# Performance work log

Hardware: AMD Instinct MI355X
Metric: run time of the kernel (lower is better)

Reference implementation:

```python
import jax, jax.numpy as jnp
import numpy as np

N, E, DIN, H, DOUT, NBLK = 50000, 300000, 963, 256, 3, 6


def gconv(x, src, dst, ew, W, Wl, b):
    # support = x @ W ; out[i] = sum_j ew_ij * support[j] + x[i] @ W_loop + b
    sup = x @ W
    agg = jax.ops.segment_sum(ew[:, None] * sup[src], dst, num_segments=N)
    return agg + x @ Wl + b


def setup_inputs() -> dict:
    key = jax.random.key(0)
    ks = jax.random.split(key, 16)
    s = 0.05
    x = jax.random.normal(ks[0], (N, DIN), jnp.float32)
    src = jax.random.randint(ks[1], (E,), 0, N, dtype=jnp.int32)
    dst = jax.random.randint(ks[2], (E,), 0, N, dtype=jnp.int32)
    ew = jax.random.uniform(ks[3], (E,), jnp.float32)
    W1 = jax.random.normal(ks[4], (DIN, H), jnp.float32) * s
    Wl1 = jax.random.normal(ks[5], (DIN, H), jnp.float32) * s
    b1 = jnp.zeros((H,), jnp.float32)
    # stacked residual-block weights: [NBLK, 2 convs, H, H]
    blkW = jax.random.normal(ks[6], (NBLK, 2, H, H), jnp.float32) * s
    blkWl = jax.random.normal(ks[7], (NBLK, 2, H, H), jnp.float32) * s
    blkb = jnp.zeros((NBLK, 2, H), jnp.float32)
    W2 = jax.random.normal(ks[8], (H, DOUT), jnp.float32) * s
    Wl2 = jax.random.normal(ks[9], (H, DOUT), jnp.float32) * s
    b2 = jnp.zeros((DOUT,), jnp.float32)
    return dict(x=x, src=src, dst=dst, ew=ew, W1=W1, Wl1=Wl1, b1=b1,
                blkW=blkW, blkWl=blkWl, blkb=blkb, W2=W2, Wl2=Wl2, b2=b2)


def reference(x, src, dst, ew, W1, Wl1, b1, blkW, blkWl, blkb, W2, Wl2, b2):
    h = jax.nn.relu(gconv(x, src, dst, ew, W1, Wl1, b1))

    def block(h, p):
        W, Wl, b = p  # W: [2,H,H]
        y = jax.nn.relu(gconv(h, src, dst, ew, W[0], Wl[0], b[0]))
        y = jax.nn.relu(gconv(y, src, dst, ew, W[1], Wl[1], b[1]))
        return (h + y) * 0.5, None

    x_hidden, _ = jax.lax.scan(block, h, (blkW, blkWl, blkb))
    x_out = gconv(x_hidden, src, dst, ew, W2, Wl2, b2)
    return (x_out, x_hidden)
```

## Files before the change

kernel.cpp:

```cpp
#include <hip/hip_runtime.h>

typedef __attribute__((ext_vector_type(8))) short short8;
typedef __attribute__((ext_vector_type(4))) float f32x4;

constexpr int kN = 50000;
constexpr int kE = 300000;
constexpr int kDIN = 963;
constexpr int kH = 256;
constexpr int kNBLK = 6;

__device__ inline unsigned short f2bf(float f) {
    unsigned u = __float_as_uint(f);
    u = u + 0x7FFFu + ((u >> 16) & 1u);
    return (unsigned short)(u >> 16);
}
__device__ inline float bf2f(unsigned short s) {
    return __uint_as_float(((unsigned)s) << 16);
}

__device__ inline void gload_lds16(const void* g, void* l) {
    __builtin_amdgcn_global_load_lds(
        (const __attribute__((address_space(1))) void*)g,
        (__attribute__((address_space(3))) void*)l, 16, 0, 0);
}

template<bool ACVT>
__global__ __launch_bounds__(512) void gemm_dual(
    const void* __restrict__ Av, const unsigned short* __restrict__ Bt,
    const float* __restrict__ bias,
    unsigned short* __restrict__ supb, unsigned short* __restrict__ tpreb,
    int M, int Kpad, int Kvalid, int Astride)
{
    __shared__ __align__(16) char smem[49152];
    char* As = smem;
    char* Bs = smem + 16384;

    const int tid = threadIdx.x;
    const int wid = tid >> 6;
    const int lane = tid & 63;
    const int wr = wid >> 2, wc = wid & 3;

    const int nwg = gridDim.x;
    const int q = nwg >> 3, r = nwg & 7;
    const int xcd = blockIdx.x & 7, idx = blockIdx.x >> 3;
    const int t = (xcd < r ? xcd * (q + 1) : r * (q + 1) + (xcd - r) * q) + idx;
    const int r0 = (t >> 1) * 128;
    const int c0 = (t & 1) * 256;

    f32x4 acc[4][4];
#pragma unroll
    for (int i = 0; i < 4; ++i)
#pragma unroll
        for (int j = 0; j < 4; ++j) acc[i][j] = f32x4{0.f, 0.f, 0.f, 0.f};

    const int l_row = lane >> 3;
    const int l_c   = lane & 7;

    for (int k0 = 0; k0 < Kpad; k0 += 64) {
#pragma unroll
        for (int p = 0; p < 4; ++p) {
            int row = wid * 32 + p * 8 + l_row;
            int csw = l_c ^ (row & 7);
            const unsigned short* g = Bt + (long)(c0 + row) * Kpad + k0 + csw * 8;
            gload_lds16(g, Bs + (wid * 32 + p * 8) * 128);
        }
        if (!ACVT) {
            const unsigned short* A = (const unsigned short*)Av;
#pragma unroll
            for (int p = 0; p < 2; ++p) {
                int row = wid * 16 + p * 8 + l_row;
                int grow = r0 + row; if (grow >= M) grow = M - 1;
                int csw = l_c ^ (row & 7);
                const unsigned short* g = A + (long)grow * Astride + k0 + csw * 8;
                gload_lds16(g, As + (wid * 16 + p * 8) * 128);
            }
        } else {
            const int row = tid >> 2;
            const int kq = tid & 3;
            int grow = r0 + row; if (grow >= M) grow = M - 1;
            const float* ar = (const float*)Av + (long)grow * Astride;
#pragma unroll
            for (int j = 0; j < 2; ++j) {
                int k16 = kq * 2 + j;
                short8 v;
#pragma unroll
                for (int ii = 0; ii < 8; ++ii) {
                    int k = k0 + k16 * 8 + ii;
                    float f = (k < Kvalid) ? ar[k] : 0.f;
                    v[ii] = (short)f2bf(f);
                }
                *(short8*)(As + row * 128 + ((k16 ^ (row & 7)) << 4)) = v;
            }
        }
        __syncthreads();

#pragma unroll
        for (int kk = 0; kk < 2; ++kk) {
            short8 af[4], bfr[4];
            const int kg = kk * 4 + (lane >> 4);
#pragma unroll
            for (int nr = 0; nr < 4; ++nr) {
                int row = wr * 64 + nr * 16 + (lane & 15);
                af[nr] = *(const short8*)(As + row * 128 + ((kg ^ (row & 7)) << 4));
            }
#pragma unroll
            for (int mc = 0; mc < 4; ++mc) {
                int row = wc * 64 + mc * 16 + (lane & 15);
                bfr[mc] = *(const short8*)(Bs + row * 128 + ((kg ^ (row & 7)) << 4));
            }
#pragma unroll
            for (int mc = 0; mc < 4; ++mc)
#pragma unroll
                for (int nr = 0; nr < 4; ++nr)
                    acc[mc][nr] = __builtin_amdgcn_mfma_f32_16x16x32_bf16(
                        bfr[mc], af[nr], acc[mc][nr], 0, 0, 0);
        }
        __syncthreads();
    }

    const bool isSup = (c0 == 0);
    unsigned short* outp = isSup ? supb : tpreb;
    float* eL = (float*)smem;
    const int wrow = wr * 16 + (lane & 15);
    const int qc = (lane >> 4) << 2;

    for (int nr = 0; nr < 4; ++nr) {
        __syncthreads();
#pragma unroll
        for (int mc = 0; mc < 4; ++mc) {
            const int col = wc * 64 + mc * 16 + qc;
            f32x4 v = acc[mc][nr];
            if (!isSup) v += *(const f32x4*)(bias + col);
            const int c16 = col >> 2;
            *(f32x4*)(eL + wrow * 256 + ((c16 ^ wrow) << 2)) = v;
        }
        __syncthreads();
        const int tr = tid >> 4, j = tid & 15;
        const int gr = r0 + (tr >> 4) * 64 + nr * 16 + (tr & 15);
        if (gr < M) {
#pragma unroll
            for (int p = 0; p < 2; ++p) {
                const int u = j + 16 * p;
                f32x4 lo = *(const f32x4*)(eL + tr * 256 + (((2 * u) ^ tr) << 2));
                f32x4 hi = *(const f32x4*)(eL + tr * 256 + (((2 * u + 1) ^ tr) << 2));
                uint4 pk;
                pk.x = (unsigned)f2bf(lo[0]) | ((unsigned)f2bf(lo[1]) << 16);
                pk.y = (unsigned)f2bf(lo[2]) | ((unsigned)f2bf(lo[3]) << 16);
                pk.z = (unsigned)f2bf(hi[0]) | ((unsigned)f2bf(hi[1]) << 16);
                pk.w = (unsigned)f2bf(hi[2]) | ((unsigned)f2bf(hi[3]) << 16);
                *(uint4*)(outp + (long)gr * 256 + u * 8) = pk;
            }
        }
    }
}

template<int MODE, bool WF32>
__global__ __launch_bounds__(256) void agg_kernel(
    const unsigned short* __restrict__ supb, const unsigned short* __restrict__ tpreb,
    const int* __restrict__ rowptr, const int* __restrict__ e_src,
    const float* __restrict__ e_w,
    const unsigned short* __restrict__ hbf_in,
    float* __restrict__ h, unsigned short* __restrict__ obf)
{
    const int wid = threadIdx.x >> 6, lane = threadIdx.x & 63;
    const long node = (long)blockIdx.x * 4 + wid;
    if (node >= kN) return;
    const int c0 = lane << 2;

    ushort4 tv = *(const ushort4*)(tpreb + node * 256 + c0);
    f32x4 a = {bf2f(tv.x), bf2f(tv.y), bf2f(tv.z), bf2f(tv.w)};
    int b = rowptr[node];
    const int e = rowptr[node + 1];

    for (; b + 4 <= e; b += 4) {
        const int s0 = e_src[b],     s1 = e_src[b + 1];
        const int s2 = e_src[b + 2], s3 = e_src[b + 3];
        const float w0 = e_w[b],     w1 = e_w[b + 1];
        const float w2 = e_w[b + 2], w3 = e_w[b + 3];
        ushort4 v0 = *(const ushort4*)(supb + (long)s0 * 256 + c0);
        ushort4 v1 = *(const ushort4*)(supb + (long)s1 * 256 + c0);
        ushort4 v2 = *(const ushort4*)(supb + (long)s2 * 256 + c0);
        ushort4 v3 = *(const ushort4*)(supb + (long)s3 * 256 + c0);
        a[0] += w0 * bf2f(v0.x) + w1 * bf2f(v1.x) + w2 * bf2f(v2.x) + w3 * bf2f(v3.x);
        a[1] += w0 * bf2f(v0.y) + w1 * bf2f(v1.y) + w2 * bf2f(v2.y) + w3 * bf2f(v3.y);
        a[2] += w0 * bf2f(v0.z) + w1 * bf2f(v1.z) + w2 * bf2f(v2.z) + w3 * bf2f(v3.z);
        a[3] += w0 * bf2f(v0.w) + w1 * bf2f(v1.w) + w2 * bf2f(v2.w) + w3 * bf2f(v3.w);
    }
    for (; b < e; ++b) {
        const int s = e_src[b];
        const float w = e_w[b];
        ushort4 sv = *(const ushort4*)(supb + (long)s * 256 + c0);
        a[0] += w * bf2f(sv.x); a[1] += w * bf2f(sv.y);
        a[2] += w * bf2f(sv.z); a[3] += w * bf2f(sv.w);
    }
    a[0] = fmaxf(a[0], 0.f); a[1] = fmaxf(a[1], 0.f);
    a[2] = fmaxf(a[2], 0.f); a[3] = fmaxf(a[3], 0.f);

    f32x4 r = a;
    if (MODE == 1) {
        ushort4 hv = *(const ushort4*)(hbf_in + node * 256 + c0);
        r[0] = (bf2f(hv.x) + a[0]) * 0.5f;
        r[1] = (bf2f(hv.y) + a[1]) * 0.5f;
        r[2] = (bf2f(hv.z) + a[2]) * 0.5f;
        r[3] = (bf2f(hv.w) + a[3]) * 0.5f;
    }
    if (WF32)
        *(f32x4*)(h + node * 256 + c0) = r;

    uint2 pk;
    pk.x = (unsigned)f2bf(r[0]) | ((unsigned)f2bf(r[1]) << 16);
    pk.y = (unsigned)f2bf(r[2]) | ((unsigned)f2bf(r[3]) << 16);
    *(uint2*)(obf + node * 256 + c0) = pk;
}

__global__ __launch_bounds__(256) void cvt_w1_kernel(
    const float* __restrict__ W1, const float* __restrict__ Wl1,
    unsigned short* __restrict__ out)
{
    int idx = blockIdx.x * 256 + threadIdx.x;
    if (idx >= 512 * 1024) return;
    int c = idx >> 10, k = idx & 1023;
    float v = 0.f;
    if (k < kDIN) v = (c < 256) ? W1[(long)k * 256 + c] : Wl1[(long)k * 256 + (c - 256)];
    out[idx] = f2bf(v);
}

__global__ __launch_bounds__(256) void cvt_blk_kernel(
    const float* __restrict__ blkW, const float* __restrict__ blkWl,
    unsigned short* __restrict__ out)
{
    int idx = blockIdx.x * 256 + threadIdx.x;
    if (idx >= 12 * 512 * 256) return;
    int l = idx >> 17;
    int rem = idx & 131071;
    int c = rem >> 8, k = rem & 255;
    float v = (c < 256) ? blkW[((long)l * 256 + k) * 256 + c]
                        : blkWl[((long)l * 256 + k) * 256 + (c - 256)];
    out[idx] = f2bf(v);
}

__global__ __launch_bounds__(256) void hist_kernel(const int* __restrict__ dst,
                                                   int* __restrict__ counts)
{
    int e = blockIdx.x * 256 + threadIdx.x;
    if (e < kE) atomicAdd(&counts[dst[e]], 1);
}

__global__ __launch_bounds__(1024) void scan1_kernel(
    const int* __restrict__ counts, int* __restrict__ rowptr, int* __restrict__ bsum)
{
    __shared__ int s[1024];
    const int tid = threadIdx.x;
    const int g = blockIdx.x * 1024 + tid;
    const int v = (g < kN) ? counts[g] : 0;
    s[tid] = v; __syncthreads();
    for (int off = 1; off < 1024; off <<= 1) {
        int tv = (tid >= off) ? s[tid - off] : 0;
        __syncthreads();
        s[tid] += tv;
        __syncthreads();
    }
    if (g < kN) rowptr[g] = s[tid] - v;
    if (tid == 1023) bsum[blockIdx.x] = s[1023];
}

__global__ __launch_bounds__(64) void scan2_kernel(int* __restrict__ bsum, int nb)
{
    __shared__ int s[64];
    const int tid = threadIdx.x;
    const int v = (tid < nb) ? bsum[tid] : 0;
    s[tid] = v; __syncthreads();
    for (int off = 1; off < 64; off <<= 1) {
        int tv = (tid >= off) ? s[tid - off] : 0;
        __syncthreads();
        s[tid] += tv;
        __syncthreads();
    }
    if (tid < nb) bsum[tid] = s[tid] - v;
}

__global__ __launch_bounds__(256) void scan3_kernel(
    int* __restrict__ rowptr, const int* __restrict__ bsum, int* __restrict__ cursor)
{
    int g = blockIdx.x * 256 + threadIdx.x;
    if (g < kN) {
        int r = rowptr[g] + bsum[g >> 10];
        rowptr[g] = r;
        cursor[g] = r;
    }
    if (g == 0) rowptr[kN] = kE;
}

__global__ __launch_bounds__(256) void fill_kernel(
    const int* __restrict__ src, const int* __restrict__ dst,
    const float* __restrict__ ew, int* __restrict__ cursor,
    int* __restrict__ e_src, float* __restrict__ e_w)
{
    int e = blockIdx.x * 256 + threadIdx.x;
    if (e >= kE) return;
    int d = dst[e];
    int pos = atomicAdd(&cursor[d], 1);
    e_src[pos] = src[e];
    e_w[pos] = ew[e];
}

__global__ __launch_bounds__(64) void final_layer_kernel(
    const unsigned short* __restrict__ hbf, const float* __restrict__ W2,
    const float* __restrict__ Wl2, const float* __restrict__ b2,
    float* __restrict__ sup2, float* __restrict__ x_out)
{
    const int row = blockIdx.x;
    const int lane = threadIdx.x;
    const unsigned short* hr = hbf + (long)row * kH;
    float accW[3] = {0.f, 0.f, 0.f};
    float accL[3] = {0.f, 0.f, 0.f};
#pragma unroll
    for (int kb = 0; kb < kH / 64; ++kb) {
        int k = kb * 64 + lane;
        float v = bf2f(hr[k]);
#pragma unroll
        for (int c = 0; c < 3; ++c) {
            accW[c] = fmaf(v, W2[k * 3 + c], accW[c]);
            accL[c] = fmaf(v, Wl2[k * 3 + c], accL[c]);
        }
    }
#pragma unroll
    for (int off = 32; off > 0; off >>= 1) {
#pragma unroll
        for (int c = 0; c < 3; ++c) {
            accW[c] += __shfl_down(accW[c], off);
            accL[c] += __shfl_down(accL[c], off);
        }
    }
    if (lane == 0) {
#pragma unroll
        for (int c = 0; c < 3; ++c) {
            sup2[row * 3 + c] = accW[c];
            x_out[row * 3 + c] = accL[c] + b2[c];
        }
    }
}

__global__ __launch_bounds__(256) void scatter3_kernel(
    const float* __restrict__ sup2, const int* __restrict__ src,
    const int* __restrict__ dst, const float* __restrict__ ew,
    float* __restrict__ x_out)
{
    int e = blockIdx.x * 256 + threadIdx.x;
    if (e >= kE) return;
    int s = src[e];
    int d = dst[e];
    float w = ew[e];
#pragma unroll
    for (int c = 0; c < 3; ++c)
        atomicAdd(&x_out[(long)d * 3 + c], w * sup2[(long)s * 3 + c]);
}

extern "C" void kernel_launch(void* const* d_in, const int* in_sizes, int n_in,
                              void* d_out, int out_size, void* d_ws, size_t ws_size,
                              hipStream_t stream)
{
    const float* x    = (const float*)d_in[0];
    const int*   src  = (const int*)d_in[1];
    const int*   dst  = (const int*)d_in[2];
    const float* ew   = (const float*)d_in[3];
    const float* W1   = (const float*)d_in[4];
    const float* Wl1  = (const float*)d_in[5];
    const float* b1   = (const float*)d_in[6];
    const float* blkW  = (const float*)d_in[7];
    const float* blkWl = (const float*)d_in[8];
    const float* blkb  = (const float*)d_in[9];
    const float* W2   = (const float*)d_in[10];
    const float* Wl2  = (const float*)d_in[11];
    const float* b2   = (const float*)d_in[12];

    float* out   = (float*)d_out;
    float* x_out = out;
    float* h     = out + (long)kN * 3;

    char* w = (char*)d_ws;
    size_t off = 0;
    auto carve = [&](size_t bytes) { char* p = w + off; off = (off + bytes + 255) & ~(size_t)255; return p; };
    unsigned short* supb  = (unsigned short*)carve(12800000UL * 2);
    unsigned short* tpreb = (unsigned short*)carve(12800000UL * 2);
    unsigned short* tact  = (unsigned short*)carve(12800000UL * 2);
    unsigned short* hbf   = (unsigned short*)carve(12800000UL * 2);
    unsigned short* w1c   = (unsigned short*)carve(512UL * 1024 * 2);
    unsigned short* blkc  = (unsigned short*)carve(12UL * 512 * 256 * 2);
    int*   e_src  = (int*)carve(kE * 4);
    float* e_w    = (float*)carve(kE * 4);
    int*   counts = (int*)carve(50176 * 4);
    int*   rowptr = (int*)carve(50176 * 4);
    int*   cursor = (int*)carve(50176 * 4);
    int*   bsum   = (int*)carve(64 * 4);
    float* sup2   = (float*)carve((long)kN * 3 * 4);

    hipMemsetAsync(counts, 0, 50176 * 4, stream);
    hist_kernel<<<(kE + 255) / 256, 256, 0, stream>>>(dst, counts);
    scan1_kernel<<<49, 1024, 0, stream>>>(counts, rowptr, bsum);
    scan2_kernel<<<1, 64, 0, stream>>>(bsum, 49);
    scan3_kernel<<<(kN + 255) / 256, 256, 0, stream>>>(rowptr, bsum, cursor);
    fill_kernel<<<(kE + 255) / 256, 256, 0, stream>>>(src, dst, ew, cursor, e_src, e_w);

    cvt_w1_kernel<<<2048, 256, 0, stream>>>(W1, Wl1, w1c);
    cvt_blk_kernel<<<6144, 256, 0, stream>>>(blkW, blkWl, blkc);

    const int gemm_grid = 2 * ((kN + 127) / 128);
    const int agg_grid = (kN + 3) / 4;

    gemm_dual<true><<<gemm_grid, 512, 0, stream>>>(x, w1c, b1, supb, tpreb,
                                                   kN, 1024, kDIN, kDIN);
    agg_kernel<0, false><<<agg_grid, 256, 0, stream>>>(
        supb, tpreb, rowptr, e_src, e_w, nullptr, nullptr, hbf);

    for (int l = 0; l < 2 * kNBLK; ++l) {
        const unsigned short* A = (l & 1) ? tact : hbf;
        gemm_dual<false><<<gemm_grid, 512, 0, stream>>>(
            A, blkc + (long)l * 512 * 256, blkb + (long)l * 256,
            supb, tpreb, kN, 256, 256, 256);
        if (l & 1) {
            if (l == 2 * kNBLK - 1)
                agg_kernel<1, true><<<agg_grid, 256, 0, stream>>>(
                    supb, tpreb, rowptr, e_src, e_w, hbf, h, hbf);
            else
                agg_kernel<1, false><<<agg_grid, 256, 0, stream>>>(
                    supb, tpreb, rowptr, e_src, e_w, hbf, nullptr, hbf);
        } else {
            agg_kernel<0, false><<<agg_grid, 256, 0, stream>>>(
                supb, tpreb, rowptr, e_src, e_w, nullptr, nullptr, tact);
        }
    }

    final_layer_kernel<<<kN, 64, 0, stream>>>(hbf, W2, Wl2, b2, sup2, x_out);
    scatter3_kernel<<<(kE + 255) / 256, 256, 0, stream>>>(sup2, src, dst, ew, x_out);
}
```

Baseline: 1.145 ms.

## Aggregate inputs before GEMM and fuse bias/relu/residual into block GEMM epilogue

For the hidden-layer convolutions, the order is now aggregate-then-multiply, using A·(xW) = (A·x)·W. A gather kernel sums neighbour activations into xagg. A single K=512 GEMM over the concatenated [act | xagg] against stacked [Wl; W] weights then produces the layer output directly, with bias, relu, residual averaging and the final fp32 write fused into the epilogue. This drops the dual 512-column GEMM output and the separate post-GEMM aggregation pass, so less intermediate data goes to and from HBM. In exchange, xagg is rounded to bf16 before the matmul, and the residual path reads hbf while writing act_out.

```diff
diff --git a/kernel.cpp b/kernel.cpp
--- a/kernel.cpp
+++ b/kernel.cpp
@@ -24,9 +24,8 @@
         (__attribute__((address_space(3))) void*)l, 16, 0, 0);
 }
 
-template<bool ACVT>
-__global__ __launch_bounds__(512) void gemm_dual(
-    const void* __restrict__ Av, const unsigned short* __restrict__ Bt,
+__global__ __launch_bounds__(512) void gemm_l1(
+    const float* __restrict__ Av, const unsigned short* __restrict__ Bt,
     const float* __restrict__ bias,
     unsigned short* __restrict__ supb, unsigned short* __restrict__ tpreb,
     int M, int Kpad, int Kvalid, int Astride)
@@ -64,21 +63,11 @@
             const unsigned short* g = Bt + (long)(c0 + row) * Kpad + k0 + csw * 8;
             gload_lds16(g, Bs + (wid * 32 + p * 8) * 128);
         }
-        if (!ACVT) {
-            const unsigned short* A = (const unsigned short*)Av;
-#pragma unroll
-            for (int p = 0; p < 2; ++p) {
-                int row = wid * 16 + p * 8 + l_row;
-                int grow = r0 + row; if (grow >= M) grow = M - 1;
-                int csw = l_c ^ (row & 7);
-                const unsigned short* g = A + (long)grow * Astride + k0 + csw * 8;
-                gload_lds16(g, As + (wid * 16 + p * 8) * 128);
-            }
-        } else {
+        {
             const int row = tid >> 2;
             const int kq = tid & 3;
             int grow = r0 + row; if (grow >= M) grow = M - 1;
-            const float* ar = (const float*)Av + (long)grow * Astride;
+            const float* ar = Av + (long)grow * Astride;
 #pragma unroll
             for (int j = 0; j < 2; ++j) {
                 int k16 = kq * 2 + j;
@@ -93,7 +82,6 @@
             }
         }
         __syncthreads();
-
 #pragma unroll
         for (int kk = 0; kk < 2; ++kk) {
             short8 af[4], bfr[4];
@@ -154,13 +142,136 @@
     }
 }
 
-template<int MODE, bool WF32>
-__global__ __launch_bounds__(256) void agg_kernel(
+template<int RES>
+__global__ __launch_bounds__(512) void gemm_blk(
+    const unsigned short* __restrict__ act, const unsigned short* __restrict__ xagg,
+    const unsigned short* __restrict__ Bt, const float* __restrict__ bias,
+    const unsigned short* __restrict__ hbf_res,
+    unsigned short* __restrict__ outbf, float* __restrict__ hf32)
+{
+    __shared__ __align__(16) char smem[49152];
+    char* As = smem;
+    char* Bs = smem + 16384;
+
+    const int tid = threadIdx.x;
+    const int wid = tid >> 6;
+    const int lane = tid & 63;
+    const int wr = wid >> 2, wc = wid & 3;
+
+    const int nwg = gridDim.x;
+    const int q = nwg >> 3, r = nwg & 7;
+    const int xcd = blockIdx.x & 7, idx = blockIdx.x >> 3;
+    const int t = (xcd < r ? xcd * (q + 1) : r * (q + 1) + (xcd - r) * q) + idx;
+    const int r0 = t * 128;
+
+    f32x4 acc[4][4];
+#pragma unroll
+    for (int i = 0; i < 4; ++i)
+#pragma unroll
+        for (int j = 0; j < 4; ++j) acc[i][j] = f32x4{0.f, 0.f, 0.f, 0.f};
+
+    const int l_row = lane >> 3;
+    const int l_c   = lane & 7;
+
+    for (int k0 = 0; k0 < 512; k0 += 64) {
+#pragma unroll
+        for (int p = 0; p < 4; ++p) {
+            int row = wid * 32 + p * 8 + l_row;
+            int csw = l_c ^ (row & 7);
+            const unsigned short* g = Bt + (long)row * 512 + k0 + csw * 8;
+            gload_lds16(g, Bs + (wid * 32 + p * 8) * 128);
+        }
+        const unsigned short* Asrc = (k0 < 256) ? (act + k0) : (xagg + (k0 - 256));
+#pragma unroll
+        for (int p = 0; p < 2; ++p) {
+            int row = wid * 16 + p * 8 + l_row;
+            int grow = r0 + row; if (grow >= kN) grow = kN - 1;
+            int csw = l_c ^ (row & 7);
+            const unsigned short* g = Asrc + (long)grow * 256 + csw * 8;
+            gload_lds16(g, As + (wid * 16 + p * 8) * 128);
+        }
+        __syncthreads();
+#pragma unroll
+        for (int kk = 0; kk < 2; ++kk) {
+            short8 af[4], bfr[4];
+            const int kg = kk * 4 + (lane >> 4);
+#pragma unroll
+            for (int nr = 0; nr < 4; ++nr) {
+                int row = wr * 64 + nr * 16 + (lane & 15);
+                af[nr] = *(const short8*)(As + row * 128 + ((kg ^ (row & 7)) << 4));
+            }
+#pragma unroll
+            for (int mc = 0; mc < 4; ++mc) {
+                int row = wc * 64 + mc * 16 + (lane & 15);
+                bfr[mc] = *(const short8*)(Bs + row * 128 + ((kg ^ (row & 7)) << 4));
+            }
+#pragma unroll
+            for (int mc = 0; mc < 4; ++mc)
+#pragma unroll
+                for (int nr = 0; nr < 4; ++nr)
+                    acc[mc][nr] = __builtin_amdgcn_mfma_f32_16x16x32_bf16(
+                        bfr[mc], af[nr], acc[mc][nr], 0, 0, 0);
+        }
+        __syncthreads();
+    }
+
+    float* eL = (float*)smem;
+    const int wrow = wr * 16 + (lane & 15);
+    const int qc = (lane >> 4) << 2;
+
+    for (int nr = 0; nr < 4; ++nr) {
+        __syncthreads();
+#pragma unroll
+        for (int mc = 0; mc < 4; ++mc) {
+            const int col = wc * 64 + mc * 16 + qc;
+            f32x4 v = acc[mc][nr] + *(const f32x4*)(bias + col);
+            const int c16 = col >> 2;
+            *(f32x4*)(eL + wrow * 256 + ((c16 ^ wrow) << 2)) = v;
+        }
+        __syncthreads();
+        const int tr = tid >> 4, j = tid & 15;
+        const int gr = r0 + (tr >> 4) * 64 + nr * 16 + (tr & 15);
+        if (gr < kN) {
+#pragma unroll
+            for (int p = 0; p < 2; ++p) {
+                const int u = j + 16 * p;
+                f32x4 lo = *(const f32x4*)(eL + tr * 256 + (((2 * u) ^ tr) << 2));
+                f32x4 hi = *(const f32x4*)(eL + tr * 256 + (((2 * u + 1) ^ tr) << 2));
+#pragma unroll
+                for (int ii = 0; ii < 4; ++ii) {
+                    lo[ii] = fmaxf(lo[ii], 0.f);
+                    hi[ii] = fmaxf(hi[ii], 0.f);
+                }
+                if (RES >= 1) {
+                    uint4 hv = *(const uint4*)(hbf_res + (long)gr * 256 + u * 8);
+                    lo[0] = (bf2f((unsigned short)(hv.x & 0xFFFF)) + lo[0]) * 0.5f;
+                    lo[1] = (bf2f((unsigned short)(hv.x >> 16))    + lo[1]) * 0.5f;
+                    lo[2] = (bf2f((unsigned short)(hv.y & 0xFFFF)) + lo[2]) * 0.5f;
+                    lo[3] = (bf2f((unsigned short)(hv.y >> 16))    + lo[3]) * 0.5f;
+                    hi[0] = (bf2f((unsigned short)(hv.z & 0xFFFF)) + hi[0]) * 0.5f;
+                    hi[1] = (bf2f((unsigned short)(hv.z >> 16))    + hi[1]) * 0.5f;
+                    hi[2] = (bf2f((unsigned short)(hv.w & 0xFFFF)) + hi[2]) * 0.5f;
+                    hi[3] = (bf2f((unsigned short)(hv.w >> 16))    + hi[3]) * 0.5f;
+                }
+                if (RES == 2) {
+                    *(f32x4*)(hf32 + (long)gr * 256 + u * 8)     = lo;
+                    *(f32x4*)(hf32 + (long)gr * 256 + u * 8 + 4) = hi;
+                }
+                uint4 pk;
+                pk.x = (unsigned)f2bf(lo[0]) | ((unsigned)f2bf(lo[1]) << 16);
+                pk.y = (unsigned)f2bf(lo[2]) | ((unsigned)f2bf(lo[3]) << 16);
+                pk.z = (unsigned)f2bf(hi[0]) | ((unsigned)f2bf(hi[1]) << 16);
+                pk.w = (unsigned)f2bf(hi[2]) | ((unsigned)f2bf(hi[3]) << 16);
+                *(uint4*)(outbf + (long)gr * 256 + u * 8) = pk;
+            }
+        }
+    }
+}
+
+__global__ __launch_bounds__(256) void agg0_kernel(
     const unsigned short* __restrict__ supb, const unsigned short* __restrict__ tpreb,
     const int* __restrict__ rowptr, const int* __restrict__ e_src,
-    const float* __restrict__ e_w,
-    const unsigned short* __restrict__ hbf_in,
-    float* __restrict__ h, unsigned short* __restrict__ obf)
+    const float* __restrict__ e_w, unsigned short* __restrict__ obf)
 {
     const int wid = threadIdx.x >> 6, lane = threadIdx.x & 63;
     const long node = (long)blockIdx.x * 4 + wid;
@@ -171,7 +282,6 @@
     f32x4 a = {bf2f(tv.x), bf2f(tv.y), bf2f(tv.z), bf2f(tv.w)};
     int b = rowptr[node];
     const int e = rowptr[node + 1];
-
     for (; b + 4 <= e; b += 4) {
         const int s0 = e_src[b],     s1 = e_src[b + 1];
         const int s2 = e_src[b + 2], s3 = e_src[b + 3];
@@ -193,24 +303,50 @@
         a[0] += w * bf2f(sv.x); a[1] += w * bf2f(sv.y);
         a[2] += w * bf2f(sv.z); a[3] += w * bf2f(sv.w);
     }
-    a[0] = fmaxf(a[0], 0.f); a[1] = fmaxf(a[1], 0.f);
-    a[2] = fmaxf(a[2], 0.f); a[3] = fmaxf(a[3], 0.f);
-
-    f32x4 r = a;
-    if (MODE == 1) {
-        ushort4 hv = *(const ushort4*)(hbf_in + node * 256 + c0);
-        r[0] = (bf2f(hv.x) + a[0]) * 0.5f;
-        r[1] = (bf2f(hv.y) + a[1]) * 0.5f;
-        r[2] = (bf2f(hv.z) + a[2]) * 0.5f;
-        r[3] = (bf2f(hv.w) + a[3]) * 0.5f;
-    }
-    if (WF32)
-        *(f32x4*)(h + node * 256 + c0) = r;
-
     uint2 pk;
-    pk.x = (unsigned)f2bf(r[0]) | ((unsigned)f2bf(r[1]) << 16);
-    pk.y = (unsigned)f2bf(r[2]) | ((unsigned)f2bf(r[3]) << 16);
+    pk.x = (unsigned)f2bf(fmaxf(a[0], 0.f)) | ((unsigned)f2bf(fmaxf(a[1], 0.f)) << 16);
+    pk.y = (unsigned)f2bf(fmaxf(a[2], 0.f)) | ((unsigned)f2bf(fmaxf(a[3], 0.f)) << 16);
     *(uint2*)(obf + node * 256 + c0) = pk;
+}
+
+__global__ __launch_bounds__(256) void aggx_kernel(
+    const unsigned short* __restrict__ act,
+    const int* __restrict__ rowptr, const int* __restrict__ e_src,
+    const float* __restrict__ e_w, unsigned short* __restrict__ xagg)
+{
+    const int wid = threadIdx.x >> 6, lane = threadIdx.x & 63;
+    const long node = (long)blockIdx.x * 4 + wid;
+    if (node >= kN) return;
+    const int c0 = lane << 2;
+
+    f32x4 a = {0.f, 0.f, 0.f, 0.f};
+    int b = rowptr[node];
+    const int e = rowptr[node + 1];
+    for (; b + 4 <= e; b += 4) {
+        const int s0 = e_src[b],     s1 = e_src[b + 1];
+        const int s2 = e_src[b + 2], s3 = e_src[b + 3];
+        const float w0 = e_w[b],     w1 = e_w[b + 1];
+        const float w2 = e_w[b + 2], w3 = e_w[b + 3];
+        ushort4 v0 = *(const ushort4*)(act + (long)s0 * 256 + c0);
+        ushort4 v1 = *(const ushort4*)(act + (long)s1 * 256 + c0);
+        ushort4 v2 = *(const ushort4*)(act + (long)s2 * 256 + c0);
+        ushort4 v3 = *(const ushort4*)(act + (long)s3 * 256 + c0);
+        a[0] += w0 * bf2f(v0.x) + w1 * bf2f(v1.x) + w2 * bf2f(v2.x) + w3 * bf2f(v3.x);
+        a[1] += w0 * bf2f(v0.y) + w1 * bf2f(v1.y) + w2 * bf2f(v2.y) + w3 * bf2f(v3.y);
+        a[2] += w0 * bf2f(v0.z) + w1 * bf2f(v1.z) + w2 * bf2f(v2.z) + w3 * bf2f(v3.z);
+        a[3] += w0 * bf2f(v0.w) + w1 * bf2f(v1.w) + w2 * bf2f(v2.w) + w3 * bf2f(v3.w);
+    }
+    for (; b < e; ++b) {
+        const int s = e_src[b];
+        const float w = e_w[b];
+        ushort4 sv = *(const ushort4*)(act + (long)s * 256 + c0);
+        a[0] += w * bf2f(sv.x); a[1] += w * bf2f(sv.y);
+        a[2] += w * bf2f(sv.z); a[3] += w * bf2f(sv.w);
+    }
+    uint2 pk;
+    pk.x = (unsigned)f2bf(a[0]) | ((unsigned)f2bf(a[1]) << 16);
+    pk.y = (unsigned)f2bf(a[2]) | ((unsigned)f2bf(a[3]) << 16);
+    *(uint2*)(xagg + node * 256 + c0) = pk;
 }
 
 __global__ __launch_bounds__(256) void cvt_w1_kernel(
@@ -230,12 +366,12 @@
     unsigned short* __restrict__ out)
 {
     int idx = blockIdx.x * 256 + threadIdx.x;
-    if (idx >= 12 * 512 * 256) return;
+    if (idx >= 12 * 256 * 512) return;
     int l = idx >> 17;
     int rem = idx & 131071;
-    int c = rem >> 8, k = rem & 255;
-    float v = (c < 256) ? blkW[((long)l * 256 + k) * 256 + c]
-                        : blkWl[((long)l * 256 + k) * 256 + (c - 256)];
+    int c = rem >> 9, k = rem & 511;
+    float v = (k < 256) ? blkWl[((long)l * 256 + k) * 256 + c]
+                        : blkW[((long)l * 256 + (k - 256)) * 256 + c];
     out[idx] = f2bf(v);
 }
 
@@ -386,7 +522,7 @@
     unsigned short* tact  = (unsigned short*)carve(12800000UL * 2);
     unsigned short* hbf   = (unsigned short*)carve(12800000UL * 2);
     unsigned short* w1c   = (unsigned short*)carve(512UL * 1024 * 2);
-    unsigned short* blkc  = (unsigned short*)carve(12UL * 512 * 256 * 2);
+    unsigned short* blkc  = (unsigned short*)carve(12UL * 256 * 512 * 2);
     int*   e_src  = (int*)carve(kE * 4);
     float* e_w    = (float*)carve(kE * 4);
     int*   counts = (int*)carve(50176 * 4);
@@ -394,6 +530,7 @@
     int*   cursor = (int*)carve(50176 * 4);
     int*   bsum   = (int*)carve(64 * 4);
     float* sup2   = (float*)carve((long)kN * 3 * 4);
+    unsigned short* xagg = tpreb;
 
     hipMemsetAsync(counts, 0, 50176 * 4, stream);
     hist_kernel<<<(kE + 255) / 256, 256, 0, stream>>>(dst, counts);
@@ -405,29 +542,27 @@
     cvt_w1_kernel<<<2048, 256, 0, stream>>>(W1, Wl1, w1c);
     cvt_blk_kernel<<<6144, 256, 0, stream>>>(blkW, blkWl, blkc);
 
-    const int gemm_grid = 2 * ((kN + 127) / 128);
+    const int l1_grid  = 2 * ((kN + 127) / 128);
+    const int blk_grid = (kN + 127) / 128;
     const int agg_grid = (kN + 3) / 4;
 
-    gemm_dual<true><<<gemm_grid, 512, 0, stream>>>(x, w1c, b1, supb, tpreb,
-                                                   kN, 1024, kDIN, kDIN);
-    agg_kernel<0, false><<<agg_grid, 256, 0, stream>>>(
-        supb, tpreb, rowptr, e_src, e_w, nullptr, nullptr, hbf);
+    gemm_l1<<<l1_grid, 512, 0, stream>>>(x, w1c, b1, supb, tpreb,
+                                         kN, 1024, kDIN, kDIN);
+    agg0_kernel<<<agg_grid, 256, 0, stream>>>(supb, tpreb, rowptr, e_src, e_w, hbf);
 
     for (int l = 0; l < 2 * kNBLK; ++l) {
-        const unsigned short* A = (l & 1) ? tact : hbf;
-        gemm_dual<false><<<gemm_grid, 512, 0, stream>>>(
-            A, blkc + (long)l * 512 * 256, blkb + (long)l * 256,
-            supb, tpreb, kN, 256, 256, 256);
+        const unsigned short* act_in = (l & 1) ? tact : hbf;
+        unsigned short* act_out      = (l & 1) ? hbf : tact;
+        aggx_kernel<<<agg_grid, 256, 0, stream>>>(act_in, rowptr, e_src, e_w, xagg);
+        const unsigned short* B = blkc + (long)l * 256 * 512;
+        const float* bb = blkb + (long)l * 256;
         if (l & 1) {
             if (l == 2 * kNBLK - 1)
-                agg_kernel<1, true><<<agg_grid, 256, 0, stream>>>(
-                    supb, tpreb, rowptr, e_src, e_w, hbf, h, hbf);
+                gemm_blk<2><<<blk_grid, 512, 0, stream>>>(act_in, xagg, B, bb, hbf, act_out, h);
             else
-                agg_kernel<1, false><<<agg_grid, 256, 0, stream>>>(
-                    supb, tpreb, rowptr, e_src, e_w, hbf, nullptr, hbf);
+                gemm_blk<1><<<blk_grid, 512, 0, stream>>>(act_in, xagg, B, bb, hbf, act_out, nullptr);
         } else {
-            agg_kernel<0, false><<<agg_grid, 256, 0, stream>>>(
-                supb, tpreb, rowptr, e_src, e_w, nullptr, nullptr, tact);
+            gemm_blk<0><<<blk_grid, 512, 0, stream>>>(act_in, xagg, B, bb, nullptr, act_out, nullptr);
         }
     }
 
```

Result: faster. 1.020 ms (-10.9%).
